# Optimization experiments

Hardware: AMD Instinct MI355X
Metric: run time of the kernel (lower is better)

## Reference

```python
import jax, jax.numpy as jnp
import numpy as np
import math

SQRT_2_OVER_PI = 0.7978845608028654  # sqrt(2/pi)
EPS = 1e-12  # F.normalize eps


def _gelu_tanh(x):
    return 0.5 * x * (1.0 + jnp.tanh(SQRT_2_OVER_PI * (x + 0.044715 * x * x * x)))


def _l2norm(v, axis=-1):
    n = jnp.sqrt(jnp.sum(v * v, axis=axis, keepdims=True))
    return v / jnp.maximum(n, EPS)


def setup_inputs() -> dict:
    key = jax.random.key(0)
    k1, k2 = jax.random.split(key)
    B, T, D = 8, 2048, 2048
    N_TRAIN = 16
    x = jax.random.normal(k1, (B, T, D), dtype=jnp.float32)
    # ring buffer stores L2-normalized token-mean vectors
    buf = jax.random.normal(k2, (N_TRAIN, D), dtype=jnp.float32)
    train_buf = _l2norm(buf, axis=-1)
    train_mask = jnp.ones((N_TRAIN,), dtype=bool)  # steady state: buffer full
    log_tau = jnp.asarray(math.log(2.0), dtype=jnp.float32)
    log_blend_train = jnp.asarray(math.log(0.3 / 0.7), dtype=jnp.float32)
    return {
        "x": x,
        "train_buf": train_buf,
        "train_mask": train_mask,
        "log_tau": log_tau,
        "log_blend_train": log_blend_train,
    }


def reference(x, train_buf, train_mask, log_tau, log_blend_train):
    B, T, D = x.shape
    tau = jnp.exp(log_tau)
    alpha = jax.nn.sigmoid(log_blend_train)
    # elementwise tanh-GELU
    y = _gelu_tanh(x)  # (B, T, D)
    # gate path uses detached activations (y.detach() in torch)
    y_flat = jax.lax.stop_gradient(y.reshape(B * T, D))
    y_n = _l2norm(y_flat, axis=-1)            # (BT, D)
    buf_n = _l2norm(train_buf, axis=-1)       # (N, D)
    sims = y_n @ buf_n.T                      # (BT, N) skinny matmul
    sims = jnp.where(train_mask[None, :], sims, jnp.asarray(-1.0, sims.dtype))
    max_sim = jnp.max(sims, axis=-1)          # (BT,)
    gate = 1.0 - alpha + alpha * jnp.exp(-tau * max_sim)  # (BT,)
    # training mode: test-buffer gate is all ones -> combined gate == train gate
    return y * gate.reshape(B, T, 1)
```

## Files before the change

kernel.cpp:

```cpp
#include <hip/hip_runtime.h>

#define LOG2E 1.4426950408889634f

constexpr int D     = 2048;
constexpr int NB    = 16;
constexpr int TPB   = 512;
constexpr int NROWS = 16384;
constexpr int RPB   = 16;
constexpr int NBLK  = NROWS / RPB;
constexpr int NKT   = 8;

typedef short bf16x8 __attribute__((ext_vector_type(8)));
typedef float f32x4  __attribute__((ext_vector_type(4)));

__device__ __forceinline__ float gelu_tanh_f(float x) {
    const float C = 0.7978845608028654f;
    const float K = 0.044715f;
    float x2 = x * x;
    float p  = __builtin_fmaf(K, x2, 1.0f);
    float z  = C * x * p;
    float e  = __builtin_amdgcn_exp2f(z * (2.0f * LOG2E));
    float th = 1.0f - 2.0f * __builtin_amdgcn_rcpf(e + 1.0f);
    float hx = 0.5f * x;
    return __builtin_fmaf(hx, th, hx);
}

__device__ __forceinline__ unsigned bpack(float a, float b) {
    unsigned ua = __builtin_bit_cast(unsigned, a);
    unsigned ub = __builtin_bit_cast(unsigned, b);
    ua += 0x7FFFu + ((ua >> 16) & 1u);
    ub += 0x7FFFu + ((ub >> 16) & 1u);
    return (ua >> 16) | (ub & 0xFFFF0000u);
}
__device__ __forceinline__ float blo(unsigned w) {
    return __builtin_bit_cast(float, w << 16);
}
__device__ __forceinline__ float bhi(unsigned w) {
    return __builtin_bit_cast(float, w & 0xFFFF0000u);
}

__global__ void __launch_bounds__(512) bfrag_kernel(
    const float* __restrict__ buf, unsigned* __restrict__ bfrag)
{
    const int id = blockIdx.x * 512 + threadIdx.x;
    const int n  = (id >> 2) & 15;
    const int k  = ((id >> 8) << 5) + (((id >> 6) & 3) << 3) + ((id & 3) << 1);
    const float* p = buf + n * D + k;
    bfrag[id] = bpack(p[0], p[1]);
}

__global__ void __launch_bounds__(TPB) gelu_gate_kernel(
    const float* __restrict__ x,
    const unsigned* __restrict__ bfrag,
    const int* __restrict__ mask_i,
    const unsigned char* __restrict__ mask_b,
    const float* __restrict__ p_log_tau,
    const float* __restrict__ p_log_blend,
    float* __restrict__ out)
{
    __shared__ unsigned ldsY[RPB * D / 2];
    __shared__ f32x4    ldsAcc[8][64];
    __shared__ float    ldsS2[8][16];
    __shared__ float    ldsGate[16];

    const int t    = threadIdx.x;
    const int lane = t & 63;
    const int wk   = t >> 6;

    const float tau   = __builtin_amdgcn_exp2f(p_log_tau[0] * LOG2E);
    const float lbt   = p_log_blend[0];
    const float alpha = __builtin_amdgcn_rcpf(1.0f + __builtin_amdgcn_exp2f(-lbt * LOG2E));

    unsigned mbits = 0;
#pragma unroll
    for (int k = 0; k < NB; ++k) {
        bool mk = (mask_i[k] != 0) || (mask_b[k] != 0);
        mbits |= (mk ? 1u : 0u) << k;
    }

    const int row0 = blockIdx.x * RPB;
    const float4* x4   = reinterpret_cast<const float4*>(x);
    float4*       out4 = reinterpret_cast<float4*>(out);
    char* ldsYb = reinterpret_cast<char*>(ldsY);

#pragma unroll
    for (int j = 0; j < RPB; ++j) {
        float4 v = x4[(size_t)(row0 + j) * (D / 4) + t];
        uint2 w;
        w.x = bpack(gelu_tanh_f(v.x), gelu_tanh_f(v.y));
        w.y = bpack(gelu_tanh_f(v.z), gelu_tanh_f(v.w));
        const int byte = (j * 4096 + 8 * t) ^ ((j & 7) << 4);
        *reinterpret_cast<uint2*>(ldsYb + byte) = w;
    }
    __syncthreads();

    const int m    = lane & 15;
    const int kgrp = lane >> 4;
    const int swzM = (m & 7) << 4;
    const char* aBase = ldsYb + m * 4096;
    const int colB0   = wk * 512 + kgrp * 16;
    const unsigned* Bb = bfrag + wk * (NKT * 256) + lane * 4;

    f32x4 acc = {0.f, 0.f, 0.f, 0.f};
    float s2 = 0.f;
#pragma unroll
    for (int kt = 0; kt < NKT; ++kt) {
        const uint4 af = *reinterpret_cast<const uint4*>(
            aBase + ((colB0 + kt * 64) ^ swzM));
        const uint4 bq = *reinterpret_cast<const uint4*>(Bb + kt * 256);
        acc = __builtin_amdgcn_mfma_f32_16x16x32_bf16(
            __builtin_bit_cast(bf16x8, af), __builtin_bit_cast(bf16x8, bq),
            acc, 0, 0, 0);
        const unsigned ws[4] = { af.x, af.y, af.z, af.w };
#pragma unroll
        for (int c = 0; c < 4; ++c) {
            const float lo = blo(ws[c]), hi = bhi(ws[c]);
            s2 = __builtin_fmaf(lo, lo, s2);
            s2 = __builtin_fmaf(hi, hi, s2);
        }
    }
    s2 += __shfl_xor(s2, 16, 64);
    s2 += __shfl_xor(s2, 32, 64);

    ldsAcc[wk][lane] = acc;
    if (lane < 16) ldsS2[wk][lane] = s2;
    __syncthreads();

    f32x4 dt = ldsAcc[0][lane];
#pragma unroll
    for (int w = 1; w < 8; ++w) dt += ldsAcc[w][lane];

    float gate[4];
#pragma unroll
    for (int j = 0; j < 4; ++j) {
        const int r = kgrp * 4 + j;
        float s2t = ldsS2[0][r];
#pragma unroll
        for (int w = 1; w < 8; ++w) s2t += ldsS2[w][r];
        const float inv = __builtin_amdgcn_rcpf(fmaxf(__builtin_sqrtf(s2t), 1e-12f));
        float s = dt[j] * inv;
        if (!((mbits >> m) & 1u)) s = -1.0f;
        s = fmaxf(s, __shfl_xor(s, 1, 64));
        s = fmaxf(s, __shfl_xor(s, 2, 64));
        s = fmaxf(s, __shfl_xor(s, 4, 64));
        s = fmaxf(s, __shfl_xor(s, 8, 64));
        gate[j] = __builtin_fmaf(alpha, __builtin_amdgcn_exp2f(-tau * s * LOG2E),
                                 1.0f - alpha);
    }
    const int src = (lane & 12) << 2;
    const float g0 = __shfl(gate[0], src, 64);
    const float g1 = __shfl(gate[1], src, 64);
    const float g2 = __shfl(gate[2], src, 64);
    const float g3 = __shfl(gate[3], src, 64);
    const float gm = (lane & 2) ? ((lane & 1) ? g3 : g2)
                                : ((lane & 1) ? g1 : g0);
    if (t < 16) ldsGate[t] = gm;
    __syncthreads();

#pragma unroll
    for (int j = 0; j < RPB; ++j) {
        const int byte = (j * 4096 + 8 * t) ^ ((j & 7) << 4);
        const uint2 w = *reinterpret_cast<const uint2*>(ldsYb + byte);
        const float gj = ldsGate[j];
        float4 o;
        o.x = blo(w.x) * gj; o.y = bhi(w.x) * gj;
        o.z = blo(w.y) * gj; o.w = bhi(w.y) * gj;
        out4[(size_t)(row0 + j) * (D / 4) + t] = o;
    }
}

extern "C" void kernel_launch(void* const* d_in, const int* in_sizes, int n_in,
                              void* d_out, int out_size, void* d_ws, size_t ws_size,
                              hipStream_t stream) {
    const float*         x      = (const float*)d_in[0];
    const float*         buf    = (const float*)d_in[1];
    const int*           mask_i = (const int*)d_in[2];
    const unsigned char* mask_b = (const unsigned char*)d_in[2];
    const float*         lt     = (const float*)d_in[3];
    const float*         lb     = (const float*)d_in[4];
    float*               out    = (float*)d_out;
    unsigned*            bfrag  = (unsigned*)d_ws;

    bfrag_kernel<<<32, 512, 0, stream>>>(buf, bfrag);
    gelu_gate_kernel<<<NBLK, TPB, 0, stream>>>(x, bfrag, mask_i, mask_b, lt, lb, out);
}
```

Measured before the change: 58.05 us.

## Shrink blocks to four rows and keep GELU output in registers

Each block now handles 4 rows with 256 threads instead of 16 rows with 512. Each thread loads two float4 per row, keeps the packed bf16 GELU values in registers for the final scaled store, and reads the per-row gate straight from the MFMA reduction lanes. This removes the LDS reread, the gate broadcast through shared memory and one barrier, and cuts LDS per block so more blocks can be resident. In exchange, the 16-row MFMA tile is only a quarter used (rows are replicated) and there are four times as many blocks.

Result: slower. 60.07 us (+3.5%).

```diff
diff --git a/kernel.cpp b/kernel.cpp
--- a/kernel.cpp
+++ b/kernel.cpp
@@ -4,11 +4,11 @@
 
 constexpr int D     = 2048;
 constexpr int NB    = 16;
-constexpr int TPB   = 512;
+constexpr int TPB   = 256;
 constexpr int NROWS = 16384;
-constexpr int RPB   = 16;
+constexpr int RPB   = 4;
 constexpr int NBLK  = NROWS / RPB;
-constexpr int NKT   = 8;
+constexpr int NKT   = 16;
 
 typedef short bf16x8 __attribute__((ext_vector_type(8)));
 typedef float f32x4  __attribute__((ext_vector_type(4)));
@@ -59,9 +59,8 @@
     float* __restrict__ out)
 {
     __shared__ unsigned ldsY[RPB * D / 2];
-    __shared__ f32x4    ldsAcc[8][64];
-    __shared__ float    ldsS2[8][16];
-    __shared__ float    ldsGate[16];
+    __shared__ f32x4    ldsAcc[4][16];
+    __shared__ float    ldsS2[4][4];
 
     const int t    = threadIdx.x;
     const int lane = t & 63;
@@ -83,30 +82,41 @@
     float4*       out4 = reinterpret_cast<float4*>(out);
     char* ldsYb = reinterpret_cast<char*>(ldsY);
 
+    float4 v[RPB][2];
 #pragma unroll
     for (int j = 0; j < RPB; ++j) {
-        float4 v = x4[(size_t)(row0 + j) * (D / 4) + t];
-        uint2 w;
-        w.x = bpack(gelu_tanh_f(v.x), gelu_tanh_f(v.y));
-        w.y = bpack(gelu_tanh_f(v.z), gelu_tanh_f(v.w));
-        const int byte = (j * 4096 + 8 * t) ^ ((j & 7) << 4);
-        *reinterpret_cast<uint2*>(ldsYb + byte) = w;
+        v[j][0] = x4[(size_t)(row0 + j) * (D / 4) + 2 * t];
+        v[j][1] = x4[(size_t)(row0 + j) * (D / 4) + 2 * t + 1];
+    }
+    uint4 ypk[RPB];
+#pragma unroll
+    for (int j = 0; j < RPB; ++j) {
+        float y0 = gelu_tanh_f(v[j][0].x), y1 = gelu_tanh_f(v[j][0].y);
+        float y2 = gelu_tanh_f(v[j][0].z), y3 = gelu_tanh_f(v[j][0].w);
+        float y4 = gelu_tanh_f(v[j][1].x), y5 = gelu_tanh_f(v[j][1].y);
+        float y6 = gelu_tanh_f(v[j][1].z), y7 = gelu_tanh_f(v[j][1].w);
+        uint4 w;
+        w.x = bpack(y0, y1); w.y = bpack(y2, y3);
+        w.z = bpack(y4, y5); w.w = bpack(y6, y7);
+        ypk[j] = w;
+        const int byte = j * 4096 + ((16 * t) ^ (j << 6));
+        *reinterpret_cast<uint4*>(ldsYb + byte) = w;
     }
     __syncthreads();
 
     const int m    = lane & 15;
+    const int mr   = m & 3;
     const int kgrp = lane >> 4;
-    const int swzM = (m & 7) << 4;
-    const char* aBase = ldsYb + m * 4096;
-    const int colB0   = wk * 512 + kgrp * 16;
+    const char* aRow = ldsYb + mr * 4096;
+    const int swz    = mr << 6;
     const unsigned* Bb = bfrag + wk * (NKT * 256) + lane * 4;
 
     f32x4 acc = {0.f, 0.f, 0.f, 0.f};
     float s2 = 0.f;
 #pragma unroll
     for (int kt = 0; kt < NKT; ++kt) {
-        const uint4 af = *reinterpret_cast<const uint4*>(
-            aBase + ((colB0 + kt * 64) ^ swzM));
+        const int off = wk * 1024 + kt * 64 + kgrp * 16;
+        const uint4 af = *reinterpret_cast<const uint4*>(aRow + (off ^ swz));
         const uint4 bq = *reinterpret_cast<const uint4*>(Bb + kt * 256);
         acc = __builtin_amdgcn_mfma_f32_16x16x32_bf16(
             __builtin_bit_cast(bf16x8, af), __builtin_bit_cast(bf16x8, bq),
@@ -122,24 +132,22 @@
     s2 += __shfl_xor(s2, 16, 64);
     s2 += __shfl_xor(s2, 32, 64);
 
-    ldsAcc[wk][lane] = acc;
-    if (lane < 16) ldsS2[wk][lane] = s2;
+    if (lane < 16) ldsAcc[wk][lane] = acc;
+    if (lane < 4)  ldsS2[wk][lane] = s2;
     __syncthreads();
 
-    f32x4 dt = ldsAcc[0][lane];
+    const int n = lane & 15;
+    f32x4 dt = ldsAcc[0][n];
 #pragma unroll
-    for (int w = 1; w < 8; ++w) dt += ldsAcc[w][lane];
+    for (int w = 1; w < 4; ++w) dt += ldsAcc[w][n];
 
     float gate[4];
 #pragma unroll
     for (int j = 0; j < 4; ++j) {
-        const int r = kgrp * 4 + j;
-        float s2t = ldsS2[0][r];
-#pragma unroll
-        for (int w = 1; w < 8; ++w) s2t += ldsS2[w][r];
+        const float s2t = ldsS2[0][j] + ldsS2[1][j] + ldsS2[2][j] + ldsS2[3][j];
         const float inv = __builtin_amdgcn_rcpf(fmaxf(__builtin_sqrtf(s2t), 1e-12f));
         float s = dt[j] * inv;
-        if (!((mbits >> m) & 1u)) s = -1.0f;
+        if (!((mbits >> n) & 1u)) s = -1.0f;
         s = fmaxf(s, __shfl_xor(s, 1, 64));
         s = fmaxf(s, __shfl_xor(s, 2, 64));
         s = fmaxf(s, __shfl_xor(s, 4, 64));
@@ -147,25 +155,18 @@
         gate[j] = __builtin_fmaf(alpha, __builtin_amdgcn_exp2f(-tau * s * LOG2E),
                                  1.0f - alpha);
     }
-    const int src = (lane & 12) << 2;
-    const float g0 = __shfl(gate[0], src, 64);
-    const float g1 = __shfl(gate[1], src, 64);
-    const float g2 = __shfl(gate[2], src, 64);
-    const float g3 = __shfl(gate[3], src, 64);
-    const float gm = (lane & 2) ? ((lane & 1) ? g3 : g2)
-                                : ((lane & 1) ? g1 : g0);
-    if (t < 16) ldsGate[t] = gm;
-    __syncthreads();
 
 #pragma unroll
     for (int j = 0; j < RPB; ++j) {
-        const int byte = (j * 4096 + 8 * t) ^ ((j & 7) << 4);
-        const uint2 w = *reinterpret_cast<const uint2*>(ldsYb + byte);
-        const float gj = ldsGate[j];
-        float4 o;
-        o.x = blo(w.x) * gj; o.y = bhi(w.x) * gj;
-        o.z = blo(w.y) * gj; o.w = bhi(w.y) * gj;
-        out4[(size_t)(row0 + j) * (D / 4) + t] = o;
+        const uint4 w = ypk[j];
+        const float gj = gate[j];
+        float4 o1, o2;
+        o1.x = blo(w.x) * gj; o1.y = bhi(w.x) * gj;
+        o1.z = blo(w.y) * gj; o1.w = bhi(w.y) * gj;
+        o2.x = blo(w.z) * gj; o2.y = bhi(w.z) * gj;
+        o2.z = blo(w.w) * gj; o2.w = bhi(w.w) * gj;
+        out4[(size_t)(row0 + j) * (D / 4) + 2 * t]     = o1;
+        out4[(size_t)(row0 + j) * (D / 4) + 2 * t + 1] = o2;
     }
 }
 
```
